# Performance work log

Measured on AMD Instinct MI355X. Metric: run time of the kernel, lower is better.

Reference implementation:

```python
import jax, jax.numpy as jnp
import numpy as np

DIM = 1024
HEADS = 16
HEAD_DIM = DIM // HEADS
B, N = 8, 1024


def setup_inputs() -> dict:
    key = jax.random.key(0)
    ks = jax.random.split(key, 10)
    s = lambda fan_in: 1.0 / np.sqrt(fan_in)
    return {
        "x": jax.random.normal(ks[0], (B, N, DIM), jnp.float32),
        "pose_angles": jax.random.normal(ks[1], (B, 3), jnp.float32),
        # weights stored (in, out) so y = x @ W + b (equivalent to torch Linear)
        "Wqkv": jax.random.normal(ks[2], (DIM, 3 * DIM), jnp.float32) * s(DIM),
        "bqkv": jnp.zeros((3 * DIM,), jnp.float32),
        "W1": jax.random.normal(ks[3], (3, 64), jnp.float32) * s(3),
        "b1": jnp.zeros((64,), jnp.float32),
        "W2": jax.random.normal(ks[4], (64, 3 * DIM), jnp.float32) * s(64),
        "b2": jnp.zeros((3 * DIM,), jnp.float32),
        "Wproj": jax.random.normal(ks[5], (DIM, DIM), jnp.float32) * s(DIM),
        "bproj": jnp.zeros((DIM,), jnp.float32),
    }


def reference(x, pose_angles, Wqkv, bqkv, W1, b1, W2, b2, Wproj, bproj):
    Bq, Nq, C = x.shape
    H, D = HEADS, HEAD_DIM
    # qkv projection -> [B,N,3,H,D] -> [3,B,H,N,D]
    qkv = (x @ Wqkv + bqkv).reshape(Bq, Nq, 3, H, D).transpose(2, 0, 3, 1, 4)
    q, k, v = qkv[0], qkv[1], qkv[2]
    # pose MLP: 3 -> 64 -> 3*dim, chunked into per-head biases [B,H,1,D]
    pose_emb = jax.nn.relu(pose_angles @ W1 + b1) @ W2 + b2
    pose_q, pose_k, pose_v = jnp.split(pose_emb, 3, axis=1)
    pose_q = pose_q.reshape(Bq, H, 1, D)
    pose_k = pose_k.reshape(Bq, H, 1, D)
    pose_v = pose_v.reshape(Bq, H, 1, D)
    q = q + pose_q
    k = k + pose_k
    v = v + pose_v
    scale = 1.0 / jnp.sqrt(jnp.asarray(D, x.dtype))
    attn = jax.nn.softmax(jnp.einsum("bhnd,bhmd->bhnm", q, k) * scale, axis=-1)
    # dropout is identity in eval mode
    out = jnp.einsum("bhnm,bhmd->bhnd", attn, v)
    out = out.transpose(0, 2, 1, 3).reshape(Bq, Nq, C)
    return out @ Wproj + bproj
```

## Files before the change

### kernel.cpp

```cpp
#include <hip/hip_runtime.h>
#include <stdint.h>

typedef unsigned short u16;
typedef short bf16x8 __attribute__((ext_vector_type(8)));
typedef short bf16x4 __attribute__((ext_vector_type(4)));
typedef float f32x4 __attribute__((ext_vector_type(4)));
typedef u16 u16x4 __attribute__((ext_vector_type(4)));

__device__ __forceinline__ u16 f2bf(float f) {
  union { float f; unsigned int u; } v; v.f = f;
  unsigned int r = v.u + 0x7fffu + ((v.u >> 16) & 1u);
  return (u16)(r >> 16);
}

__device__ __forceinline__ void async16(const void* g, void* l) {
  __builtin_amdgcn_global_load_lds(
      (const __attribute__((address_space(1))) unsigned int*)g,
      (__attribute__((address_space(3))) unsigned int*)l, 16, 0, 0);
}

__device__ __forceinline__ f32x4 mfma16x16(bf16x4 a, bf16x4 b, f32x4 c) {
#if __has_builtin(__builtin_amdgcn_mfma_f32_16x16x16bf16_1k)
  return __builtin_amdgcn_mfma_f32_16x16x16bf16_1k(a, b, c, 0, 0, 0);
#else
  asm volatile("v_mfma_f32_16x16x16_bf16 %0, %1, %2, %0\n\ts_nop 7\n\ts_nop 7"
               : "+v"(c) : "v"(a), "v"(b));
  return c;
#endif
}

__global__ void pose_mlp_kernel(const float* __restrict__ ang, const float* __restrict__ W1,
                                const float* __restrict__ b1, const float* __restrict__ W2,
                                const float* __restrict__ b2, float* __restrict__ pose) {
  __shared__ float hid[8][64];
  int t = threadIdx.x;
  for (int idx = t; idx < 512; idx += 256) {
    int b = idx >> 6, j = idx & 63;
    float a = b1[j];
#pragma unroll
    for (int i = 0; i < 3; ++i) a += ang[b * 3 + i] * W1[i * 64 + j];
    hid[b][j] = fmaxf(a, 0.f);
  }
  __syncthreads();
  int idx = blockIdx.x * 256 + t;
  int b = idx / 3072, c = idx - b * 3072;
  float a = b2[c];
#pragma unroll
  for (int j = 0; j < 64; ++j) a += hid[b][j] * W2[j * 3072 + c];
  pose[idx] = a;
}

__global__ void cast_x_kernel(const float4* __restrict__ x, u16x4* __restrict__ y, int n4) {
  int i = blockIdx.x * blockDim.x + threadIdx.x;
  const int stride = gridDim.x * blockDim.x;
  for (; i < n4; i += stride) {
    float4 v = x[i];
    u16x4 o;
    o[0] = f2bf(v.x); o[1] = f2bf(v.y); o[2] = f2bf(v.z); o[3] = f2bf(v.w);
    y[i] = o;
  }
}

__global__ void transpose_cast_kernel(const float* __restrict__ W, u16* __restrict__ Wt,
                                      int Kdim, int Ncol) {
  __shared__ float tile[64][65];
  const int tx = threadIdx.x, ty = threadIdx.y;
  const int c0 = blockIdx.x * 64, k0 = blockIdx.y * 64;
#pragma unroll
  for (int rr = 0; rr < 16; ++rr) {
    int row = rr * 4 + ty;
    tile[row][tx] = W[(size_t)(k0 + row) * Ncol + c0 + tx];
  }
  __syncthreads();
#pragma unroll
  for (int rr = 0; rr < 16; ++rr) {
    int row = rr * 4 + ty;
    Wt[(size_t)(c0 + row) * Kdim + k0 + tx] = f2bf(tile[tx][row]);
  }
}

template <int EPI, int NJF>
__global__ void __launch_bounds__(512) gemm8_kernel(
    const u16* __restrict__ A, const u16* __restrict__ Bt,
    const float* __restrict__ bias, const float* __restrict__ pose,
    u16* __restrict__ qout, u16* __restrict__ kout, u16* __restrict__ vtout,
    float* __restrict__ cout, int Kdim, int Ncols, int nTilesX) {
  constexpr int BN = NJF * 64;
  constexpr int NJH = NJF / 2;
  constexpr int NST = 2 + NJF / 2;
  constexpr int BOFF = 256 * 64;
  __shared__ u16 lds[2][(256 + BN) * 64];
  const int t = threadIdx.x, l = t & 63, w = t >> 6;
  const int g = l >> 4, r16 = l & 15;
  const int wr = w >> 2, wc = w & 3;
  const int xk = r16 & 7;
  const int nwg = gridDim.x, cpx = nwg >> 3;
  const int swz = (blockIdx.x & 7) * cpx + (blockIdx.x >> 3);
  const int n0 = (swz % nTilesX) * BN, m0 = (swz / nTilesX) * 256;
  const u16* Ab = A + (size_t)m0 * Kdim;
  const u16* Bb = Bt + (size_t)n0 * Kdim;

  auto stage = [&](int buf, int kt, int st) {
#pragma unroll
    for (int it = 0; it < 2; ++it) {
      int idx = it * 512 + t;
      int row = idx >> 3;
      int seg = (idx & 7) ^ (row & 7);
      if (st < 2) {
        async16(Ab + (size_t)(st * 128 + row) * Kdim + kt + seg * 8,
                &lds[buf][st * 128 * 64 + idx * 8]);
      } else {
        async16(Bb + (size_t)((st - 2) * 128 + row) * Kdim + kt + seg * 8,
                &lds[buf][BOFF + (st - 2) * 128 * 64 + idx * 8]);
      }
    }
  };

  f32x4 acc[8][NJF] = {};
  const int nT = Kdim >> 6;
#pragma unroll
  for (int st = 0; st < NST; ++st) stage(0, 0, st);

  for (int tt = 0; tt < nT; ++tt) {
    const int cur = tt & 1, nxt = cur ^ 1;
    const bool pf = (tt + 1 < nT);
    const int ktn = (tt + 1) << 6;
#pragma unroll
    for (int ph = 0; ph < 4; ++ph) {
      const int mh = ph >> 1, nh = ph & 1;
      if (ph == 0) {
        if (pf) {
          stage(nxt, ktn, 0);
          __builtin_amdgcn_sched_barrier(0);
          asm volatile("s_waitcnt vmcnt(2)" ::: "memory");
        } else {
          asm volatile("s_waitcnt vmcnt(0)" ::: "memory");
        }
        __builtin_amdgcn_s_barrier();
        __builtin_amdgcn_sched_barrier(0);
      } else {
        if (pf && ph < NST) stage(nxt, ktn, ph);
      }
      bf16x8 af[4][2], bfr[NJH][2];
#pragma unroll
      for (int mi2 = 0; mi2 < 4; ++mi2)
#pragma unroll
        for (int ks = 0; ks < 2; ++ks) {
          int arow = wr * 128 + (mh * 4 + mi2) * 16 + r16;
          af[mi2][ks] = *(const bf16x8*)&lds[cur][arow * 64 + (((ks * 4 + g) ^ xk)) * 8];
        }
#pragma unroll
      for (int nj2 = 0; nj2 < NJH; ++nj2)
#pragma unroll
        for (int ks = 0; ks < 2; ++ks) {
          int brow = wc * (NJF * 16) + (nh * NJH + nj2) * 16 + r16;
          bfr[nj2][ks] = *(const bf16x8*)&lds[cur][BOFF + brow * 64 + (((ks * 4 + g) ^ xk)) * 8];
        }
      if (ph != 0) __builtin_amdgcn_s_barrier();
      __builtin_amdgcn_s_setprio(1);
#pragma unroll
      for (int ks = 0; ks < 2; ++ks)
#pragma unroll
        for (int mi2 = 0; mi2 < 4; ++mi2)
#pragma unroll
          for (int nj2 = 0; nj2 < NJH; ++nj2)
            acc[mh * 4 + mi2][nh * NJH + nj2] = __builtin_amdgcn_mfma_f32_16x16x32_bf16(
                af[mi2][ks], bfr[nj2][ks], acc[mh * 4 + mi2][nh * NJH + nj2], 0, 0, 0);
      __builtin_amdgcn_s_setprio(0);
      __builtin_amdgcn_s_barrier();
    }
  }

#pragma unroll
  for (int mi = 0; mi < 8; ++mi)
#pragma unroll
    for (int nj = 0; nj < NJF; ++nj)
#pragma unroll
      for (int r = 0; r < 4; ++r) {
        int row = m0 + wr * 128 + mi * 16 + g * 4 + r;
        int col = n0 + wc * (NJF * 16) + nj * 16 + r16;
        float v = acc[mi][nj][r] + bias[col];
        if (EPI == 0) {
          int b = row >> 10, n = row & 1023;
          v += pose[b * 3072 + col];
          u16 hv = f2bf(v);
          int three = col >> 10, hh = (col >> 6) & 15, d = col & 63;
          size_t bhh = (size_t)(b * 16 + hh);
          if (three == 0)      qout[(bhh * 1024 + n) * 64 + d] = hv;
          else if (three == 1) kout[(bhh * 1024 + n) * 64 + d] = hv;
          else                 vtout[(bhh * 64 + d) * 1024 + n] = hv;
        } else {
          cout[(size_t)row * Ncols + col] = v;
        }
      }
}

__global__ void __launch_bounds__(256) attn_kernel(
    const u16* __restrict__ Qb, const u16* __restrict__ Kb,
    const u16* __restrict__ Vtb, u16* __restrict__ aout) {
  __shared__ u16 ldsK[64][72];
  __shared__ u16 ldsV[64][72];
  const int t = threadIdx.x, l = t & 63, w = t >> 6;
  const int g = l >> 4, r16 = l & 15;
  const int bh = blockIdx.x >> 4, qt = blockIdx.x & 15;
  const int b = bh >> 4, h = bh & 15;
  const int q0 = qt * 64 + w * 16;
  const u16* Qp = Qb + ((size_t)bh * 1024 + q0 + r16) * 64;
  bf16x8 qreg0 = *(const bf16x8*)(Qp + g * 8);
  bf16x8 qreg1 = *(const bf16x8*)(Qp + 32 + g * 8);
  const u16* Kbase = Kb + (size_t)bh * 1024 * 64;
  const u16* Vbase = Vtb + (size_t)bh * 64 * 1024;
  float m = -1e30f, rs = 0.f;
  f32x4 o[4] = {};
  for (int key0 = 0; key0 < 1024; key0 += 64) {
#pragma unroll
    for (int ii = 0; ii < 2; ++ii) {
      int idx = ii * 256 + t, row = idx >> 3, seg = idx & 7;
      *(bf16x8*)&ldsK[row][seg * 8] = *(const bf16x8*)(Kbase + (size_t)(key0 + row) * 64 + seg * 8);
      *(bf16x8*)&ldsV[row][seg * 8] = *(const bf16x8*)(Vbase + (size_t)row * 1024 + key0 + seg * 8);
    }
    __syncthreads();
    f32x4 s[4] = {};
#pragma unroll
    for (int f = 0; f < 4; ++f) {
      bf16x8 ak0 = *(const bf16x8*)&ldsK[f * 16 + r16][g * 8];
      s[f] = __builtin_amdgcn_mfma_f32_16x16x32_bf16(ak0, qreg0, s[f], 0, 0, 0);
      bf16x8 ak1 = *(const bf16x8*)&ldsK[f * 16 + r16][32 + g * 8];
      s[f] = __builtin_amdgcn_mfma_f32_16x16x32_bf16(ak1, qreg1, s[f], 0, 0, 0);
    }
    float mt = -1e30f;
#pragma unroll
    for (int f = 0; f < 4; ++f)
#pragma unroll
      for (int r = 0; r < 4; ++r) { s[f][r] *= 0.125f; mt = fmaxf(mt, s[f][r]); }
    mt = fmaxf(mt, __shfl_xor(mt, 16));
    mt = fmaxf(mt, __shfl_xor(mt, 32));
    float mnew = fmaxf(m, mt);
    float alpha = __expf(m - mnew);
    float rt = 0.f;
    bf16x4 pa[4];
#pragma unroll
    for (int f = 0; f < 4; ++f) {
#pragma unroll
      for (int r = 0; r < 4; ++r) {
        float p = __expf(s[f][r] - mnew);
        rt += p;
        pa[f][r] = (short)f2bf(p);
      }
    }
    rt += __shfl_xor(rt, 16);
    rt += __shfl_xor(rt, 32);
    rs = rs * alpha + rt;
    m = mnew;
    float ar[4];
#pragma unroll
    for (int r = 0; r < 4; ++r) ar[r] = __shfl(alpha, (l & 48) | (g * 4 + r));
#pragma unroll
    for (int nf = 0; nf < 4; ++nf)
#pragma unroll
      for (int r = 0; r < 4; ++r) o[nf][r] *= ar[r];
#pragma unroll
    for (int s4 = 0; s4 < 4; ++s4)
#pragma unroll
      for (int nf = 0; nf < 4; ++nf) {
        bf16x4 bv = *(const bf16x4*)&ldsV[nf * 16 + r16][s4 * 16 + g * 4];
        o[nf] = mfma16x16(pa[s4], bv, o[nf]);
      }
    __syncthreads();
  }
  float rr[4];
#pragma unroll
  for (int r = 0; r < 4; ++r) rr[r] = __shfl(1.0f / rs, (l & 48) | (g * 4 + r));
#pragma unroll
  for (int nf = 0; nf < 4; ++nf)
#pragma unroll
    for (int r = 0; r < 4; ++r) {
      int qq = qt * 64 + w * 16 + g * 4 + r;
      int d = nf * 16 + r16;
      aout[((size_t)b * 1024 + qq) * 1024 + h * 64 + d] = f2bf(o[nf][r] * rr[r]);
    }
}

extern "C" void kernel_launch(void* const* d_in, const int* in_sizes, int n_in,
                              void* d_out, int out_size, void* d_ws, size_t ws_size,
                              hipStream_t stream) {
  (void)in_sizes; (void)n_in; (void)out_size; (void)ws_size;
  const float* x     = (const float*)d_in[0];
  const float* ang   = (const float*)d_in[1];
  const float* Wqkv  = (const float*)d_in[2];
  const float* bqkv  = (const float*)d_in[3];
  const float* W1    = (const float*)d_in[4];
  const float* b1    = (const float*)d_in[5];
  const float* W2    = (const float*)d_in[6];
  const float* b2    = (const float*)d_in[7];
  const float* Wproj = (const float*)d_in[8];
  const float* bproj = (const float*)d_in[9];
  float* out = (float*)d_out;
  char* ws = (char*)d_ws;

  u16* xh     = (u16*)(ws);
  u16* wqkvt  = (u16*)(ws + (size_t)16 * 1024 * 1024);
  u16* wprojt = (u16*)(ws + (size_t)22 * 1024 * 1024);
  float* pose = (float*)(ws + (size_t)24 * 1024 * 1024);
  u16* Qb     = (u16*)(ws + (size_t)25 * 1024 * 1024);
  u16* Kb     = (u16*)(ws + (size_t)41 * 1024 * 1024);
  u16* Vtb    = (u16*)(ws + (size_t)57 * 1024 * 1024);

  pose_mlp_kernel<<<96, 256, 0, stream>>>(ang, W1, b1, W2, b2, pose);
  cast_x_kernel<<<2048, 256, 0, stream>>>((const float4*)x, (u16x4*)xh, 8 * 1024 * 1024 / 4);
  transpose_cast_kernel<<<dim3(48, 16), dim3(64, 4), 0, stream>>>(Wqkv, wqkvt, 1024, 3072);
  transpose_cast_kernel<<<dim3(16, 16), dim3(64, 4), 0, stream>>>(Wproj, wprojt, 1024, 1024);
  gemm8_kernel<0, 4><<<384, 512, 0, stream>>>(xh, wqkvt, bqkv, pose,
                                              Qb, Kb, Vtb, nullptr, 1024, 3072, 12);
  attn_kernel<<<2048, 256, 0, stream>>>(Qb, Kb, Vtb, xh);
  gemm8_kernel<1, 2><<<256, 512, 0, stream>>>(xh, wprojt, bproj, nullptr,
                                              nullptr, nullptr, nullptr, out, 1024, 1024, 8);
}
```

Measured before the change: 234.6 us.

## Switch GEMM to fixed 256x128 tiles with 4x2 wave grid and split prefetch

```diff
diff --git a/kernel.cpp b/kernel.cpp
--- a/kernel.cpp
+++ b/kernel.cpp
@@ -79,106 +79,107 @@
   }
 }
 
-template <int EPI, int NJF>
+template <int EPI>
 __global__ void __launch_bounds__(512) gemm8_kernel(
     const u16* __restrict__ A, const u16* __restrict__ Bt,
     const float* __restrict__ bias, const float* __restrict__ pose,
     u16* __restrict__ qout, u16* __restrict__ kout, u16* __restrict__ vtout,
     float* __restrict__ cout, int Kdim, int Ncols, int nTilesX) {
-  constexpr int BN = NJF * 64;
-  constexpr int NJH = NJF / 2;
-  constexpr int NST = 2 + NJF / 2;
   constexpr int BOFF = 256 * 64;
-  __shared__ u16 lds[2][(256 + BN) * 64];
+  __shared__ u16 lds[2][(256 + 128) * 64];
   const int t = threadIdx.x, l = t & 63, w = t >> 6;
   const int g = l >> 4, r16 = l & 15;
-  const int wr = w >> 2, wc = w & 3;
+  const int wr = w >> 1, wc = w & 1;
   const int xk = r16 & 7;
   const int nwg = gridDim.x, cpx = nwg >> 3;
   const int swz = (blockIdx.x & 7) * cpx + (blockIdx.x >> 3);
-  const int n0 = (swz % nTilesX) * BN, m0 = (swz / nTilesX) * 256;
+  const int n0 = (swz % nTilesX) * 128, m0 = (swz / nTilesX) * 256;
   const u16* Ab = A + (size_t)m0 * Kdim;
   const u16* Bb = Bt + (size_t)n0 * Kdim;
 
   auto stage = [&](int buf, int kt, int st) {
 #pragma unroll
     for (int it = 0; it < 2; ++it) {
-      int idx = it * 512 + t;
-      int row = idx >> 3;
+      int idx = it * 512 + t, row = idx >> 3;
       int seg = (idx & 7) ^ (row & 7);
-      if (st < 2) {
+      if (st < 2)
         async16(Ab + (size_t)(st * 128 + row) * Kdim + kt + seg * 8,
                 &lds[buf][st * 128 * 64 + idx * 8]);
-      } else {
-        async16(Bb + (size_t)((st - 2) * 128 + row) * Kdim + kt + seg * 8,
-                &lds[buf][BOFF + (st - 2) * 128 * 64 + idx * 8]);
-      }
+      else
+        async16(Bb + (size_t)row * Kdim + kt + seg * 8, &lds[buf][BOFF + idx * 8]);
     }
   };
 
-  f32x4 acc[8][NJF] = {};
+  f32x4 acc[4][4] = {};
   const int nT = Kdim >> 6;
 #pragma unroll
-  for (int st = 0; st < NST; ++st) stage(0, 0, st);
+  for (int st = 0; st < 3; ++st) stage(0, 0, st);
 
   for (int tt = 0; tt < nT; ++tt) {
     const int cur = tt & 1, nxt = cur ^ 1;
     const bool pf = (tt + 1 < nT);
     const int ktn = (tt + 1) << 6;
-#pragma unroll
-    for (int ph = 0; ph < 4; ++ph) {
-      const int mh = ph >> 1, nh = ph & 1;
-      if (ph == 0) {
-        if (pf) {
-          stage(nxt, ktn, 0);
-          __builtin_amdgcn_sched_barrier(0);
-          asm volatile("s_waitcnt vmcnt(2)" ::: "memory");
-        } else {
-          asm volatile("s_waitcnt vmcnt(0)" ::: "memory");
-        }
-        __builtin_amdgcn_s_barrier();
-        __builtin_amdgcn_sched_barrier(0);
-      } else {
-        if (pf && ph < NST) stage(nxt, ktn, ph);
-      }
-      bf16x8 af[4][2], bfr[NJH][2];
-#pragma unroll
-      for (int mi2 = 0; mi2 < 4; ++mi2)
-#pragma unroll
-        for (int ks = 0; ks < 2; ++ks) {
-          int arow = wr * 128 + (mh * 4 + mi2) * 16 + r16;
-          af[mi2][ks] = *(const bf16x8*)&lds[cur][arow * 64 + (((ks * 4 + g) ^ xk)) * 8];
-        }
-#pragma unroll
-      for (int nj2 = 0; nj2 < NJH; ++nj2)
-#pragma unroll
-        for (int ks = 0; ks < 2; ++ks) {
-          int brow = wc * (NJF * 16) + (nh * NJH + nj2) * 16 + r16;
-          bfr[nj2][ks] = *(const bf16x8*)&lds[cur][BOFF + brow * 64 + (((ks * 4 + g) ^ xk)) * 8];
-        }
-      if (ph != 0) __builtin_amdgcn_s_barrier();
-      __builtin_amdgcn_s_setprio(1);
+    if (pf) {
+      stage(nxt, ktn, 0);
+      __builtin_amdgcn_sched_barrier(0);
+      asm volatile("s_waitcnt vmcnt(2)" ::: "memory");
+    } else {
+      asm volatile("s_waitcnt vmcnt(0)" ::: "memory");
+    }
+    __builtin_amdgcn_s_barrier();
+    __builtin_amdgcn_sched_barrier(0);
+    bf16x8 bfr[4][2], af[2][2];
+#pragma unroll
+    for (int nj = 0; nj < 4; ++nj)
 #pragma unroll
       for (int ks = 0; ks < 2; ++ks)
-#pragma unroll
-        for (int mi2 = 0; mi2 < 4; ++mi2)
-#pragma unroll
-          for (int nj2 = 0; nj2 < NJH; ++nj2)
-            acc[mh * 4 + mi2][nh * NJH + nj2] = __builtin_amdgcn_mfma_f32_16x16x32_bf16(
-                af[mi2][ks], bfr[nj2][ks], acc[mh * 4 + mi2][nh * NJH + nj2], 0, 0, 0);
-      __builtin_amdgcn_s_setprio(0);
-      __builtin_amdgcn_s_barrier();
-    }
-  }
-
-#pragma unroll
-  for (int mi = 0; mi < 8; ++mi)
-#pragma unroll
-    for (int nj = 0; nj < NJF; ++nj)
+        bfr[nj][ks] = *(const bf16x8*)&lds[cur][BOFF + (wc * 64 + nj * 16 + r16) * 64 +
+                                               ((ks * 4 + g) ^ xk) * 8];
+#pragma unroll
+    for (int mi = 0; mi < 2; ++mi)
+#pragma unroll
+      for (int ks = 0; ks < 2; ++ks)
+        af[mi][ks] = *(const bf16x8*)&lds[cur][(wr * 64 + mi * 16 + r16) * 64 +
+                                              ((ks * 4 + g) ^ xk) * 8];
+    __builtin_amdgcn_s_setprio(1);
+#pragma unroll
+    for (int ks = 0; ks < 2; ++ks)
+#pragma unroll
+      for (int mi = 0; mi < 2; ++mi)
+#pragma unroll
+        for (int nj = 0; nj < 4; ++nj)
+          acc[mi][nj] = __builtin_amdgcn_mfma_f32_16x16x32_bf16(af[mi][ks], bfr[nj][ks],
+                                                                acc[mi][nj], 0, 0, 0);
+    __builtin_amdgcn_s_setprio(0);
+    if (pf) { stage(nxt, ktn, 1); stage(nxt, ktn, 2); }
+    bf16x8 af2[2][2];
+#pragma unroll
+    for (int mi = 0; mi < 2; ++mi)
+#pragma unroll
+      for (int ks = 0; ks < 2; ++ks)
+        af2[mi][ks] = *(const bf16x8*)&lds[cur][(wr * 64 + (mi + 2) * 16 + r16) * 64 +
+                                               ((ks * 4 + g) ^ xk) * 8];
+    __builtin_amdgcn_s_setprio(1);
+#pragma unroll
+    for (int ks = 0; ks < 2; ++ks)
+#pragma unroll
+      for (int mi = 0; mi < 2; ++mi)
+#pragma unroll
+        for (int nj = 0; nj < 4; ++nj)
+          acc[mi + 2][nj] = __builtin_amdgcn_mfma_f32_16x16x32_bf16(af2[mi][ks], bfr[nj][ks],
+                                                                    acc[mi + 2][nj], 0, 0, 0);
+    __builtin_amdgcn_s_setprio(0);
+    __builtin_amdgcn_s_barrier();
+  }
+
+#pragma unroll
+  for (int mi = 0; mi < 4; ++mi)
+#pragma unroll
+    for (int nj = 0; nj < 4; ++nj)
 #pragma unroll
       for (int r = 0; r < 4; ++r) {
-        int row = m0 + wr * 128 + mi * 16 + g * 4 + r;
-        int col = n0 + wc * (NJF * 16) + nj * 16 + r16;
+        int row = m0 + wr * 64 + mi * 16 + g * 4 + r;
+        int col = n0 + wc * 64 + nj * 16 + r16;
         float v = acc[mi][nj][r] + bias[col];
         if (EPI == 0) {
           int b = row >> 10, n = row & 1023;
@@ -310,9 +311,9 @@
   cast_x_kernel<<<2048, 256, 0, stream>>>((const float4*)x, (u16x4*)xh, 8 * 1024 * 1024 / 4);
   transpose_cast_kernel<<<dim3(48, 16), dim3(64, 4), 0, stream>>>(Wqkv, wqkvt, 1024, 3072);
   transpose_cast_kernel<<<dim3(16, 16), dim3(64, 4), 0, stream>>>(Wproj, wprojt, 1024, 1024);
-  gemm8_kernel<0, 4><<<384, 512, 0, stream>>>(xh, wqkvt, bqkv, pose,
-                                              Qb, Kb, Vtb, nullptr, 1024, 3072, 12);
+  gemm8_kernel<0><<<768, 512, 0, stream>>>(xh, wqkvt, bqkv, pose,
+                                           Qb, Kb, Vtb, nullptr, 1024, 3072, 24);
   attn_kernel<<<2048, 256, 0, stream>>>(Qb, Kb, Vtb, xh);
-  gemm8_kernel<1, 2><<<256, 512, 0, stream>>>(xh, wprojt, bproj, nullptr,
-                                              nullptr, nullptr, nullptr, out, 1024, 1024, 8);
-}
+  gemm8_kernel<1><<<256, 512, 0, stream>>>(xh, wprojt, bproj, nullptr,
+                                           nullptr, nullptr, nullptr, out, 1024, 1024, 8);
+}
```

Result: faster. 207.8 us (-11.4%).
